# Performance work log

Measured on AMD Instinct MI355X. Metric: run time of the kernel, lower is better.

The kernel has to match this reference:

```python
import jax, jax.numpy as jnp
import numpy as np

N, E, D, H, G, C = 100000, 1200000, 64, 64, 128, 10


def setup_inputs() -> dict:
    key = jax.random.key(0)
    ks = jax.random.split(key, 20)
    def lin(k, fin, fout):
        kw, kb = jax.random.split(k)
        s = 1.0 / np.sqrt(fin)
        return (jax.random.uniform(kw, (fin, fout), jnp.float32, -s, s),
                jax.random.uniform(kb, (fout,), jnp.float32, -s, s))
    w1a, b1a = lin(ks[0], D, H)
    w1b, b1b = lin(ks[1], H, H)
    w2a, b2a = lin(ks[2], H, H)
    w2b, b2b = lin(ks[3], H, H)
    w3a, b3a = lin(ks[4], H, H)
    w3b, b3b = lin(ks[5], H, H)
    wc, bc = lin(ks[6], H, C)
    x = jax.random.normal(ks[7], (N, D), jnp.float32)
    edge_index = jax.random.randint(ks[8], (2, E), 0, N, dtype=jnp.int32)
    batch = jnp.sort(jax.random.randint(ks[9], (N,), 0, G, dtype=jnp.int32))
    return {"x": x, "w1a": w1a, "b1a": b1a, "w1b": w1b, "b1b": b1b,
            "w2a": w2a, "b2a": b2a, "w2b": w2b, "b2b": b2b,
            "w3a": w3a, "b3a": b3a, "w3b": w3b, "b3b": b3b,
            "wc": wc, "bc": bc, "edge_index": edge_index, "batch": batch}


def _gin_layer(x, src, dst, wa, ba, wb, bb):
    # GINConv (eps=0): mlp(x + sum_{j in N(i)} x_j), then outer ReLU from GIN.forward
    agg = jax.ops.segment_sum(x[src], dst, num_segments=N)  # [N, d]
    h = x + agg
    h = jax.nn.relu(h @ wa + ba) @ wb + bb
    return jax.nn.relu(h)


def reference(x, w1a, b1a, w1b, b1b, w2a, b2a, w2b, b2b,
              w3a, b3a, w3b, b3b, wc, bc, edge_index, batch):
    src, dst = edge_index[0], edge_index[1]
    x = _gin_layer(x, src, dst, w1a, b1a, w1b, b1b)
    x = _gin_layer(x, src, dst, w2a, b2a, w2b, b2b)
    x = _gin_layer(x, src, dst, w3a, b3a, w3b, b3b)
    # global mean pool over graphs
    sums = jax.ops.segment_sum(x, batch, num_segments=G)              # [G, H]
    cnts = jax.ops.segment_sum(jnp.ones((N,), x.dtype), batch, num_segments=G)
    pooled = sums / jnp.maximum(cnts, 1.0)[:, None]
    return pooled @ wc + bc  # [G, C]
```

## Files before the change

kernel.cpp:

```cpp
#include <hip/hip_runtime.h>
#include <hip/hip_bf16.h>


#define N_NODES 100000
#define N_EDGES 1200000
#define N_GRAPH 128
#define N_CLS   10
#define NBUCK   391
#define BCAP    4096
#define BSH     12

typedef __bf16 bf16_t;
typedef __bf16 bf16x8 __attribute__((ext_vector_type(8)));
typedef float  f32x4  __attribute__((ext_vector_type(4)));

__global__ void tobf_kernel(const float* __restrict__ x, bf16_t* __restrict__ xb,
                            int* __restrict__ bcnt, float* __restrict__ gsum,
                            const float* __restrict__ w1a, const float* __restrict__ w1b,
                            const float* __restrict__ w2a, const float* __restrict__ w2b,
                            const float* __restrict__ w3a, const float* __restrict__ w3b,
                            bf16_t* __restrict__ wfragG) {
    const int tid = threadIdx.x;
    if (blockIdx.x == 0) {
        for (int i = tid; i < NBUCK; i += 256) bcnt[i] = 0;
    } else if (blockIdx.x == 1) {
        f32x4* g4 = (f32x4*)gsum;
        for (int i = tid; i < N_GRAPH * 16; i += 256)
            g4[i] = (f32x4){0.f, 0.f, 0.f, 0.f};
    } else if (blockIdx.x <= 4) {
        const int L = blockIdx.x - 2;
        const float* wA = L == 0 ? w1a : (L == 1 ? w2a : w3a);
        const float* wB = L == 0 ? w1b : (L == 1 ? w2b : w3b);
        const int k  = tid >> 2;
        const int n0 = (tid & 3) << 4;
        const int ks = k >> 5, qd = (k >> 3) & 3, jj = k & 7;
        const int fi = ((n0 >> 4) << 1) + ks;
#pragma unroll
        for (int m = 0; m < 2; ++m) {
            const float* w = m ? wB : wA;
            const f32x4 v0 = *(const f32x4*)(w + k * 64 + n0);
            const f32x4 v1 = *(const f32x4*)(w + k * 64 + n0 + 4);
            const f32x4 v2 = *(const f32x4*)(w + k * 64 + n0 + 8);
            const f32x4 v3 = *(const f32x4*)(w + k * 64 + n0 + 12);
            bf16_t* dst = wfragG + ((L * 2 + m) * 8 + fi) * 512 + jj;
#pragma unroll
            for (int l = 0; l < 4; ++l) {
                dst[(qd * 16 + l) * 8]      = (bf16_t)v0[l];
                dst[(qd * 16 + 4 + l) * 8]  = (bf16_t)v1[l];
                dst[(qd * 16 + 8 + l) * 8]  = (bf16_t)v2[l];
                dst[(qd * 16 + 12 + l) * 8] = (bf16_t)v3[l];
            }
        }
    }
    const int i = (blockIdx.x * 256 + tid) * 8;
    const f32x4 a = *(const f32x4*)(x + i);
    const f32x4 b = *(const f32x4*)(x + i + 4);
    bf16x8 o;
#pragma unroll
    for (int j = 0; j < 4; ++j) { o[j] = (bf16_t)a[j]; o[4 + j] = (bf16_t)b[j]; }
    *(bf16x8*)(xb + i) = o;
}

__global__ void binA_kernel(const int* __restrict__ ei,
                            int* __restrict__ bcnt,
                            int* __restrict__ bpair) {
    __shared__ int lcnt[NBUCK];
    __shared__ int lbase[NBUCK];
    const int t = threadIdx.x;
    for (int b = t; b < NBUCK; b += 256) lcnt[b] = 0;
    __syncthreads();
    const int e0 = (blockIdx.x * 256 + t) * 4;
    int4 s4, d4; int b[4], r[4];
    const bool valid = e0 < N_EDGES;
    if (valid) {
        s4 = *(const int4*)(ei + e0);
        d4 = *(const int4*)(ei + N_EDGES + e0);
        b[0] = d4.x >> 8; b[1] = d4.y >> 8; b[2] = d4.z >> 8; b[3] = d4.w >> 8;
        r[0] = atomicAdd(&lcnt[b[0]], 1);
        r[1] = atomicAdd(&lcnt[b[1]], 1);
        r[2] = atomicAdd(&lcnt[b[2]], 1);
        r[3] = atomicAdd(&lcnt[b[3]], 1);
    }
    __syncthreads();
    for (int bb = t; bb < NBUCK; bb += 256) {
        const int c = lcnt[bb];
        lbase[bb] = c ? atomicAdd(&bcnt[bb], c) : 0;
    }
    __syncthreads();
    if (valid) {
        const int ss[4] = {s4.x, s4.y, s4.z, s4.w};
        const int dd[4] = {d4.x, d4.y, d4.z, d4.w};
#pragma unroll
        for (int j = 0; j < 4; ++j) {
            const int slot = lbase[b[j]] + r[j];
            if (slot < BCAP)
                bpair[(b[j] << BSH) + slot] = (ss[j] << 8) | (dd[j] & 255);
        }
    }
}

__global__ void sortfill_kernel(const int* __restrict__ bpair,
                                const int* __restrict__ bcnt,
                                int* __restrict__ offset, int* __restrict__ csr) {
    __shared__ int red[256];
    __shared__ int hist[256];
    __shared__ int l[256];
    __shared__ int cursor[256];
    const int b = blockIdx.x;
    const int t = threadIdx.x;
    const int base = b << BSH;

    int part = 0;
    for (int i = t; i < b; i += 256) {
        int c = bcnt[i];
        part += (c < BCAP ? c : BCAP);
    }
    red[t] = part;
    __syncthreads();
    for (int d = 128; d > 0; d >>= 1) {
        if (t < d) red[t] += red[t + d];
        __syncthreads();
    }
    const int cbase = red[0];
    int cnt = bcnt[b];
    cnt = cnt < BCAP ? cnt : BCAP;
    if (b == NBUCK - 1 && t == 0) offset[N_NODES] = cbase + cnt;
    __syncthreads();

    hist[t] = 0;
    __syncthreads();
    for (int i = t; i < cnt; i += 256)
        atomicAdd(&hist[bpair[base + i] & 255], 1);
    __syncthreads();

    const int v = hist[t];
    l[t] = v;
    __syncthreads();
    for (int d = 1; d < 256; d <<= 1) {
        int u = l[t];
        if (t >= d) u += l[t - d];
        __syncthreads();
        l[t] = u;
        __syncthreads();
    }
    const int gpos = cbase + l[t] - v;
    const int node = (b << 8) + t;
    if (node < N_NODES) offset[node] = gpos;
    cursor[t] = gpos;
    __syncthreads();

    for (int i = t; i < cnt; i += 256) {
        const int p = bpair[base + i];
        const int pos = atomicAdd(&cursor[p & 255], 1);
        csr[pos] = p >> 8;
    }
}

#define GATHER8(S, J, ACC)                                                     \
    {                                                                          \
        const int t0 = __shfl(S, J + 0), t1 = __shfl(S, J + 1);                \
        const int t2 = __shfl(S, J + 2), t3 = __shfl(S, J + 3);                \
        const int t4 = __shfl(S, J + 4), t5 = __shfl(S, J + 5);                \
        const int t6 = __shfl(S, J + 6), t7 = __shfl(S, J + 7);                \
        const float u0 = (float)x[t0 * 64 + f], u1 = (float)x[t1 * 64 + f];    \
        const float u2 = (float)x[t2 * 64 + f], u3 = (float)x[t3 * 64 + f];    \
        const float u4 = (float)x[t4 * 64 + f], u5 = (float)x[t5 * 64 + f];    \
        const float u6 = (float)x[t6 * 64 + f], u7 = (float)x[t7 * 64 + f];    \
        ACC += ((u0 + u1) + (u2 + u3)) + ((u4 + u5) + (u6 + u7));              \
    }
#define GATHER4(S, J, ACC)                                                     \
    {                                                                          \
        const int t0 = __shfl(S, J + 0), t1 = __shfl(S, J + 1);                \
        const int t2 = __shfl(S, J + 2), t3 = __shfl(S, J + 3);                \
        const float u0 = (float)x[t0 * 64 + f], u1 = (float)x[t1 * 64 + f];    \
        const float u2 = (float)x[t2 * 64 + f], u3 = (float)x[t3 * 64 + f];    \
        ACC += (u0 + u1) + (u2 + u3);                                          \
    }

template <int POOL>
__global__ void gmlp_kernel(const bf16_t* __restrict__ x,
                            const int* __restrict__ offset,
                            const int* __restrict__ csr,
                            const bf16_t* __restrict__ wf,
                            const float* __restrict__ ba, const float* __restrict__ bb,
                            bf16_t* __restrict__ xout,
                            const int* __restrict__ batch,
                            float* __restrict__ gsum) {
    __shared__ __align__(16) bf16_t hs[16][72];
    __shared__ __align__(16) bf16_t h2[16][72];

    const int tid  = threadIdx.x;
    const int half = tid >> 6;
    const int lane = tid & 63;
    const int l15  = lane & 15;
    const int quad = lane >> 4;

    const int rb  = blockIdx.x * 16;
    const int r0w = rb + half * 8;
    const int f   = lane;

    int offv = 0;
    if (lane < 9) offv = offset[r0w + lane];

    for (int i = 0; i < 4; ++i) {
        const int nA = r0w + i;
        const int nB = r0w + i + 4;
        const int oA = __shfl(offv, i),     eA = __shfl(offv, i + 1);
        const int oB = __shfl(offv, i + 4), eB = __shfl(offv, i + 5);
        const int dA = eA - oA, dB = eB - oB;

        float accA = (float)x[nA * 64 + f];
        float accB = (float)x[nB * 64 + f];

        for (int base = 0; base < dA || base < dB; base += 64) {
            const int ra = dA - base, rb2 = dB - base;
            const int cntA = ra <= 0 ? 0 : (ra < 64 ? ra : 64);
            const int cntB = rb2 <= 0 ? 0 : (rb2 < 64 ? rb2 : 64);
            int sA = 0, sB = 0;
            if (f < cntA) sA = csr[oA + base + f];
            if (f < cntB) sB = csr[oB + base + f];

            int j = 0;
            for (; j + 8 <= cntA && j + 8 <= cntB; j += 8) {
                GATHER8(sA, j, accA)
                GATHER8(sB, j, accB)
            }
            int jA = j, jB = j;
            for (; jA + 8 <= cntA; jA += 8) { GATHER8(sA, jA, accA) }
            for (; jB + 8 <= cntB; jB += 8) { GATHER8(sB, jB, accB) }
            if (jA + 4 <= cntA && jB + 4 <= cntB) {
                GATHER4(sA, jA, accA)
                GATHER4(sB, jB, accB)
                jA += 4; jB += 4;
            }
            if (jA + 4 <= cntA) { GATHER4(sA, jA, accA) jA += 4; }
            if (jB + 4 <= cntB) { GATHER4(sB, jB, accB) jB += 4; }
            for (; jA < cntA; ++jA) { const int t = __shfl(sA, jA); accA += (float)x[t * 64 + f]; }
            for (; jB < cntB; ++jB) { const int t = __shfl(sB, jB); accB += (float)x[t * 64 + f]; }
        }
        hs[half * 8 + i][lane]     = (bf16_t)accA;
        hs[half * 8 + i + 4][lane] = (bf16_t)accB;
    }

    __syncthreads();

    {
        bf16x8 af[2];
#pragma unroll
        for (int ks = 0; ks < 2; ++ks)
            af[ks] = *(const bf16x8*)(&hs[l15][ks * 32 + quad * 8]);
#pragma unroll
        for (int c = 0; c < 2; ++c) {
            const int ct = half * 2 + c;
            const bf16x8 b0 = *(const bf16x8*)(wf + (0 * 8 + ct * 2 + 0) * 512 + lane * 8);
            const bf16x8 b1 = *(const bf16x8*)(wf + (0 * 8 + ct * 2 + 1) * 512 + lane * 8);
            f32x4 acc = {0.f, 0.f, 0.f, 0.f};
            acc = __builtin_amdgcn_mfma_f32_16x16x32_bf16(af[0], b0, acc, 0, 0, 0);
            acc = __builtin_amdgcn_mfma_f32_16x16x32_bf16(af[1], b1, acc, 0, 0, 0);
            const float bv = ba[ct * 16 + l15];
#pragma unroll
            for (int r = 0; r < 4; ++r) {
                float h = acc[r] + bv;
                h = h > 0.f ? h : 0.f;
                h2[quad * 4 + r][ct * 16 + l15] = (bf16_t)h;
            }
        }
    }

    __syncthreads();

    {
        bf16x8 a2[2];
#pragma unroll
        for (int ks = 0; ks < 2; ++ks)
            a2[ks] = *(const bf16x8*)(&h2[l15][ks * 32 + quad * 8]);
#pragma unroll
        for (int c = 0; c < 2; ++c) {
            const int ct = half * 2 + c;
            const bf16x8 b0 = *(const bf16x8*)(wf + (1 * 8 + ct * 2 + 0) * 512 + lane * 8);
            const bf16x8 b1 = *(const bf16x8*)(wf + (1 * 8 + ct * 2 + 1) * 512 + lane * 8);
            f32x4 acc = {0.f, 0.f, 0.f, 0.f};
            acc = __builtin_amdgcn_mfma_f32_16x16x32_bf16(a2[0], b0, acc, 0, 0, 0);
            acc = __builtin_amdgcn_mfma_f32_16x16x32_bf16(a2[1], b1, acc, 0, 0, 0);
            const float bv = bb[ct * 16 + l15];
#pragma unroll
            for (int r = 0; r < 4; ++r) {
                float h = acc[r] + bv;
                h = h > 0.f ? h : 0.f;
                hs[quad * 4 + r][ct * 16 + l15] = (bf16_t)h;
            }
        }
    }

    __syncthreads();

    if (POOL) {
        int cur = -1;
        float acc = 0.f;
        for (int r = 0; r < 8; ++r) {
            const int row = r0w + r;
            const int g = batch[row];
            const float v = (float)hs[half * 8 + r][lane];
            if (g != cur) {
                if (cur >= 0) unsafeAtomicAdd(gsum + cur * 64 + lane, acc);
                acc = 0.f;
                cur = g;
            }
            acc += v;
        }
        if (cur >= 0) unsafeAtomicAdd(gsum + cur * 64 + lane, acc);
    } else {
        const int row16 = half * 8 + (lane >> 3);
        const int colg  = (lane & 7) * 8;
        const bf16x8 v = *(const bf16x8*)&hs[row16][colg];
        *(bf16x8*)(xout + (rb + row16) * 64 + colg) = v;
    }
}

__global__ void cls_kernel(const float* __restrict__ gsum,
                           const int* __restrict__ batch,
                           const float* __restrict__ wc, const float* __restrict__ bc,
                           float* __restrict__ out) {
    const int g = blockIdx.x;
    const int c = threadIdx.x;
    if (c >= N_CLS) return;
    int lo = 0, hi = N_NODES;
    while (lo < hi) { const int m = (lo + hi) >> 1; if (batch[m] < g) lo = m + 1; else hi = m; }
    const int lb = lo;
    lo = 0; hi = N_NODES;
    while (lo < hi) { const int m = (lo + hi) >> 1; if (batch[m] <= g) lo = m + 1; else hi = m; }
    const int cnt = lo - lb;
    const float inv = 1.f / (float)(cnt > 1 ? cnt : 1);
    float acc = bc[c];
    for (int k = 0; k < 64; ++k)
        acc += gsum[g * 64 + k] * inv * wc[k * N_CLS + c];
    out[g * N_CLS + c] = acc;
}

extern "C" void kernel_launch(void* const* d_in, const int* in_sizes, int n_in,
                              void* d_out, int out_size, void* d_ws, size_t ws_size,
                              hipStream_t stream) {
    const float* x   = (const float*)d_in[0];
    const float* w1a = (const float*)d_in[1];
    const float* b1a = (const float*)d_in[2];
    const float* w1b = (const float*)d_in[3];
    const float* b1b = (const float*)d_in[4];
    const float* w2a = (const float*)d_in[5];
    const float* b2a = (const float*)d_in[6];
    const float* w2b = (const float*)d_in[7];
    const float* b2b = (const float*)d_in[8];
    const float* w3a = (const float*)d_in[9];
    const float* b3a = (const float*)d_in[10];
    const float* w3b = (const float*)d_in[11];
    const float* b3b = (const float*)d_in[12];
    const float* wc  = (const float*)d_in[13];
    const float* bc  = (const float*)d_in[14];
    const int*   ei    = (const int*)d_in[15];
    const int*   batch = (const int*)d_in[16];
    float* out = (float*)d_out;

    char*   ws     = (char*)d_ws;
    int*    bcnt   = (int*)ws;
    int*    offset = (int*)(ws + 3136);
    int*    csr    = (int*)(ws + 403152);
    int*    bpair  = (int*)(ws + 5203152);
    bf16_t* xbf    = (bf16_t*)(ws + 11609296);
    bf16_t* h      = (bf16_t*)(ws + 24409296);
    bf16_t* xA     = (bf16_t*)(ws + 37209296);
    float*  gsum   = (float*)(ws + 50009296);
    bf16_t* wfragG = (bf16_t*)(ws + 50042064);

    const int e4grid = (N_EDGES / 4 + 255) / 256;
    const int tiles  = N_NODES / 16;

    tobf_kernel<<<(N_NODES * 64) / (256 * 8), 256, 0, stream>>>(
        x, xbf, bcnt, gsum, w1a, w1b, w2a, w2b, w3a, w3b, wfragG);

    binA_kernel<<<e4grid, 256, 0, stream>>>(ei, bcnt, bpair);
    sortfill_kernel<<<NBUCK, 256, 0, stream>>>(bpair, bcnt, offset, csr);

    gmlp_kernel<0><<<tiles, 128, 0, stream>>>(xbf, offset, csr, wfragG,        b1a, b1b, xA, nullptr, nullptr);
    gmlp_kernel<0><<<tiles, 128, 0, stream>>>(xA,  offset, csr, wfragG + 8192, b2a, b2b, h,  nullptr, nullptr);
    gmlp_kernel<1><<<tiles, 128, 0, stream>>>(h,   offset, csr, wfragG + 16384, b3a, b3b, nullptr, batch, gsum);

    cls_kernel<<<N_GRAPH, 64, 0, stream>>>(gsum, batch, wc, bc, out);
}
```

Baseline: 296.1 us.

## Pad gather with zero sentinel row and prefetch all CSR index chunks upfront

Adds a zero row at index N_NODES in each bf16 feature buffer so out-of-range neighbor slots can point to it, which lets the gather always run in groups of 8 without 4-wide or scalar tail loops. The first 64 CSR indices for all 8 rows of a wavefront are now loaded up front, before any gathers, so index loads overlap instead of being serialized per row. Rows with degree above 64 fall back to an extra chunked loop. This removes branchy tail handling at the cost of some wasted loads from the zero row and more live registers.

```diff
diff --git a/kernel.cpp b/kernel.cpp
--- a/kernel.cpp
+++ b/kernel.cpp
@@ -19,7 +19,8 @@
                             const float* __restrict__ w1a, const float* __restrict__ w1b,
                             const float* __restrict__ w2a, const float* __restrict__ w2b,
                             const float* __restrict__ w3a, const float* __restrict__ w3b,
-                            bf16_t* __restrict__ wfragG) {
+                            bf16_t* __restrict__ wfragG,
+                            bf16_t* __restrict__ hPad, bf16_t* __restrict__ xAPad) {
     const int tid = threadIdx.x;
     if (blockIdx.x == 0) {
         for (int i = tid; i < NBUCK; i += 256) bcnt[i] = 0;
@@ -27,6 +28,11 @@
         f32x4* g4 = (f32x4*)gsum;
         for (int i = tid; i < N_GRAPH * 16; i += 256)
             g4[i] = (f32x4){0.f, 0.f, 0.f, 0.f};
+        if (tid < 64) {
+            xb[N_NODES * 64 + tid]    = (bf16_t)0.f;
+            hPad[N_NODES * 64 + tid]  = (bf16_t)0.f;
+            xAPad[N_NODES * 64 + tid] = (bf16_t)0.f;
+        }
     } else if (blockIdx.x <= 4) {
         const int L = blockIdx.x - 2;
         const float* wA = L == 0 ? w1a : (L == 1 ? w2a : w3a);
@@ -156,25 +162,45 @@
     }
 }
 
-#define GATHER8(S, J, ACC)                                                     \
+#define G8(S, J, ACC)                                                          \
     {                                                                          \
-        const int t0 = __shfl(S, J + 0), t1 = __shfl(S, J + 1);                \
-        const int t2 = __shfl(S, J + 2), t3 = __shfl(S, J + 3);                \
-        const int t4 = __shfl(S, J + 4), t5 = __shfl(S, J + 5);                \
-        const int t6 = __shfl(S, J + 6), t7 = __shfl(S, J + 7);                \
+        const int t0 = __shfl(S, (J) + 0), t1 = __shfl(S, (J) + 1);            \
+        const int t2 = __shfl(S, (J) + 2), t3 = __shfl(S, (J) + 3);            \
+        const int t4 = __shfl(S, (J) + 4), t5 = __shfl(S, (J) + 5);            \
+        const int t6 = __shfl(S, (J) + 6), t7 = __shfl(S, (J) + 7);            \
         const float u0 = (float)x[t0 * 64 + f], u1 = (float)x[t1 * 64 + f];    \
         const float u2 = (float)x[t2 * 64 + f], u3 = (float)x[t3 * 64 + f];    \
         const float u4 = (float)x[t4 * 64 + f], u5 = (float)x[t5 * 64 + f];    \
         const float u6 = (float)x[t6 * 64 + f], u7 = (float)x[t7 * 64 + f];    \
         ACC += ((u0 + u1) + (u2 + u3)) + ((u4 + u5) + (u6 + u7));              \
     }
-#define GATHER4(S, J, ACC)                                                     \
+
+#define ROWPAIR(I, SA, CA, DA, OA, SB, CB, DB, OB)                             \
     {                                                                          \
-        const int t0 = __shfl(S, J + 0), t1 = __shfl(S, J + 1);                \
-        const int t2 = __shfl(S, J + 2), t3 = __shfl(S, J + 3);                \
-        const float u0 = (float)x[t0 * 64 + f], u1 = (float)x[t1 * 64 + f];    \
-        const float u2 = (float)x[t2 * 64 + f], u3 = (float)x[t3 * 64 + f];    \
-        ACC += (u0 + u1) + (u2 + u3);                                          \
+        float accA = (float)x[(r0w + I) * 64 + f];                             \
+        float accB = (float)x[(r0w + I + 4) * 64 + f];                         \
+        const int cmax = (CA) > (CB) ? (CA) : (CB);                            \
+        for (int j = 0; j < cmax; j += 8) {                                    \
+            if (j < (CA)) { G8(SA, j, accA) }                                  \
+            if (j < (CB)) { G8(SB, j, accB) }                                  \
+        }                                                                      \
+        if ((DA) > 64 || (DB) > 64) {                      \
+            for (int base = 64; base < (DA) || base < (DB); base += 64) {      \
+                const int ra = (DA) - base, rb2 = (DB) - base;                 \
+                const int ca2 = ra <= 0 ? 0 : (ra < 64 ? ra : 64);             \
+                const int cb2 = rb2 <= 0 ? 0 : (rb2 < 64 ? rb2 : 64);          \
+                int sA2 = N_NODES, sB2 = N_NODES;                              \
+                if (f < ca2) sA2 = csr[(OA) + base + f];                       \
+                if (f < cb2) sB2 = csr[(OB) + base + f];                       \
+                const int cm2 = ca2 > cb2 ? ca2 : cb2;                         \
+                for (int j = 0; j < cm2; j += 8) {                             \
+                    if (j < ca2) { G8(sA2, j, accA) }                          \
+                    if (j < cb2) { G8(sB2, j, accB) }                          \
+                }                                                              \
+            }                                                                  \
+        }                                                                      \
+        hs[half * 8 + I][lane]     = (bf16_t)accA;                             \
+        hs[half * 8 + I + 4][lane] = (bf16_t)accB;                             \
     }
 
 template <int POOL>
@@ -201,46 +227,31 @@
 
     int offv = 0;
     if (lane < 9) offv = offset[r0w + lane];
-
-    for (int i = 0; i < 4; ++i) {
-        const int nA = r0w + i;
-        const int nB = r0w + i + 4;
-        const int oA = __shfl(offv, i),     eA = __shfl(offv, i + 1);
-        const int oB = __shfl(offv, i + 4), eB = __shfl(offv, i + 5);
-        const int dA = eA - oA, dB = eB - oB;
-
-        float accA = (float)x[nA * 64 + f];
-        float accB = (float)x[nB * 64 + f];
-
-        for (int base = 0; base < dA || base < dB; base += 64) {
-            const int ra = dA - base, rb2 = dB - base;
-            const int cntA = ra <= 0 ? 0 : (ra < 64 ? ra : 64);
-            const int cntB = rb2 <= 0 ? 0 : (rb2 < 64 ? rb2 : 64);
-            int sA = 0, sB = 0;
-            if (f < cntA) sA = csr[oA + base + f];
-            if (f < cntB) sB = csr[oB + base + f];
-
-            int j = 0;
-            for (; j + 8 <= cntA && j + 8 <= cntB; j += 8) {
-                GATHER8(sA, j, accA)
-                GATHER8(sB, j, accB)
-            }
-            int jA = j, jB = j;
-            for (; jA + 8 <= cntA; jA += 8) { GATHER8(sA, jA, accA) }
-            for (; jB + 8 <= cntB; jB += 8) { GATHER8(sB, jB, accB) }
-            if (jA + 4 <= cntA && jB + 4 <= cntB) {
-                GATHER4(sA, jA, accA)
-                GATHER4(sB, jB, accB)
-                jA += 4; jB += 4;
-            }
-            if (jA + 4 <= cntA) { GATHER4(sA, jA, accA) jA += 4; }
-            if (jB + 4 <= cntB) { GATHER4(sB, jB, accB) jB += 4; }
-            for (; jA < cntA; ++jA) { const int t = __shfl(sA, jA); accA += (float)x[t * 64 + f]; }
-            for (; jB < cntB; ++jB) { const int t = __shfl(sB, jB); accB += (float)x[t * 64 + f]; }
-        }
-        hs[half * 8 + i][lane]     = (bf16_t)accA;
-        hs[half * 8 + i + 4][lane] = (bf16_t)accB;
-    }
+    const int o0 = __shfl(offv, 0), o1 = __shfl(offv, 1), o2 = __shfl(offv, 2);
+    const int o3 = __shfl(offv, 3), o4 = __shfl(offv, 4), o5 = __shfl(offv, 5);
+    const int o6 = __shfl(offv, 6), o7 = __shfl(offv, 7), o8 = __shfl(offv, 8);
+    const int d0 = o1 - o0, d1 = o2 - o1, d2 = o3 - o2, d3 = o4 - o3;
+    const int d4 = o5 - o4, d5 = o6 - o5, d6 = o7 - o6, d7 = o8 - o7;
+    const int c0 = d0 < 64 ? d0 : 64, c1 = d1 < 64 ? d1 : 64;
+    const int c2 = d2 < 64 ? d2 : 64, c3 = d3 < 64 ? d3 : 64;
+    const int c4 = d4 < 64 ? d4 : 64, c5 = d5 < 64 ? d5 : 64;
+    const int c6 = d6 < 64 ? d6 : 64, c7 = d7 < 64 ? d7 : 64;
+
+    int s0 = N_NODES, s1 = N_NODES, s2 = N_NODES, s3 = N_NODES;
+    int s4 = N_NODES, s5 = N_NODES, s6 = N_NODES, s7 = N_NODES;
+    if (f < c0) s0 = csr[o0 + f];
+    if (f < c1) s1 = csr[o1 + f];
+    if (f < c2) s2 = csr[o2 + f];
+    if (f < c3) s3 = csr[o3 + f];
+    if (f < c4) s4 = csr[o4 + f];
+    if (f < c5) s5 = csr[o5 + f];
+    if (f < c6) s6 = csr[o6 + f];
+    if (f < c7) s7 = csr[o7 + f];
+
+    ROWPAIR(0, s0, c0, d0, o0, s4, c4, d4, o4)
+    ROWPAIR(1, s1, c1, d1, o1, s5, c5, d5, o5)
+    ROWPAIR(2, s2, c2, d2, o2, s6, c6, d6, o6)
+    ROWPAIR(3, s3, c3, d3, o3, s7, c7, d7, o7)
 
     __syncthreads();
 
@@ -365,22 +376,22 @@
     int*    csr    = (int*)(ws + 403152);
     int*    bpair  = (int*)(ws + 5203152);
     bf16_t* xbf    = (bf16_t*)(ws + 11609296);
-    bf16_t* h      = (bf16_t*)(ws + 24409296);
-    bf16_t* xA     = (bf16_t*)(ws + 37209296);
-    float*  gsum   = (float*)(ws + 50009296);
-    bf16_t* wfragG = (bf16_t*)(ws + 50042064);
+    bf16_t* h      = (bf16_t*)(ws + 24409424);
+    bf16_t* xA     = (bf16_t*)(ws + 37209552);
+    float*  gsum   = (float*)(ws + 50009680);
+    bf16_t* wfragG = (bf16_t*)(ws + 50042448);
 
     const int e4grid = (N_EDGES / 4 + 255) / 256;
     const int tiles  = N_NODES / 16;
 
     tobf_kernel<<<(N_NODES * 64) / (256 * 8), 256, 0, stream>>>(
-        x, xbf, bcnt, gsum, w1a, w1b, w2a, w2b, w3a, w3b, wfragG);
+        x, xbf, bcnt, gsum, w1a, w1b, w2a, w2b, w3a, w3b, wfragG, h, xA);
 
     binA_kernel<<<e4grid, 256, 0, stream>>>(ei, bcnt, bpair);
     sortfill_kernel<<<NBUCK, 256, 0, stream>>>(bpair, bcnt, offset, csr);
 
-    gmlp_kernel<0><<<tiles, 128, 0, stream>>>(xbf, offset, csr, wfragG,        b1a, b1b, xA, nullptr, nullptr);
-    gmlp_kernel<0><<<tiles, 128, 0, stream>>>(xA,  offset, csr, wfragG + 8192, b2a, b2b, h,  nullptr, nullptr);
+    gmlp_kernel<0><<<tiles, 128, 0, stream>>>(xbf, offset, csr, wfragG,         b1a, b1b, xA, nullptr, nullptr);
+    gmlp_kernel<0><<<tiles, 128, 0, stream>>>(xA,  offset, csr, wfragG + 8192,  b2a, b2b, h,  nullptr, nullptr);
     gmlp_kernel<1><<<tiles, 128, 0, stream>>>(h,   offset, csr, wfragG + 16384, b3a, b3b, nullptr, batch, gsum);
 
     cls_kernel<<<N_GRAPH, 64, 0, stream>>>(gsum, batch, wc, bc, out);
```

Measured after the change: 287.7 us. -2.8%, faster.
